# Optimization experiments

Hardware: AMD Instinct MI355X
Metric: run time of the kernel (lower is better)

The kernel has to match this reference:

```python
import jax, jax.numpy as jnp
import numpy as np

EPS = 1e-06        # normalize eps and log eps (module's self.eps)
PDIST_EPS = 1e-06  # torch.nn.PairwiseDistance default eps: ||x1 - x2 + eps||_2

A, C, F = 4096, 8, 64


def setup_inputs() -> dict:
    key = jax.random.key(0)
    x = jax.random.normal(key, (A, C, F), dtype=jnp.float32)
    return {"x": x}


def reference(x) -> jnp.ndarray:
    a = x.shape[0]
    c = x.shape[1]
    # F.normalize(p=2, dim=-1, eps=EPS): x / max(||x||_2, eps)
    nrm = jnp.linalg.norm(x, axis=-1, keepdims=True)
    xn = x / jnp.maximum(nrm, EPS)
    # pairwise cosine similarity per group: [C, A, A]
    sim = jnp.einsum('acf,bcf->cab', xn, xn)
    # mask self-similarity on the diagonal with -1
    diag = jnp.eye(a, dtype=bool)[None, :, :]
    sim = jnp.where(diag, -1.0, sim)
    # nearest neighbor per (c, a): argmax over b -> [C, A] -> [A, C]
    idx = jnp.argmax(sim, axis=-1).T
    # gather matched embeddings: x_match[a, c, f] = xn[idx[a, c], c, f]
    x_match = xn[idx, jnp.arange(c)[None, :], :]
    # PairwiseDistance(p=2, eps=1e-6): ||x - x_match + eps||_2 over last dim
    min_dist = jnp.linalg.norm(xn - x_match + PDIST_EPS, axis=-1)
    loss = -jnp.mean(jnp.log(min_dist + EPS))
    return loss
```

## Files before the change

kernel.cpp:

```cpp
#include <hip/hip_runtime.h>
#include <math.h>

#define AN 4096
#define CN 8
#define FN 64
#define ACN (AN*CN)

typedef __attribute__((ext_vector_type(8))) short bf16x8;
typedef __attribute__((ext_vector_type(4))) float f32x4;

__device__ inline unsigned short f2bf(float f) {
    unsigned u = __float_as_uint(f);
    unsigned r = ((u >> 16) & 1) + 0x7FFFu;
    return (unsigned short)((u + r) >> 16);
}

__global__ __launch_bounds__(256) void k1_normalize(const float* __restrict__ x,
                                                    unsigned short* __restrict__ xnb,
                                                    float* __restrict__ sc)
{
    int tid  = threadIdx.x;
    int grp  = tid >> 4;
    int slot = tid & 15;
    int V = blockIdx.x * 16 + grp;
    const float4 v = *(const float4*)(x + (size_t)V * FN + slot * 4);
    float ss = v.x*v.x + v.y*v.y + v.z*v.z + v.w*v.w;
    ss += __shfl_xor(ss, 1);
    ss += __shfl_xor(ss, 2);
    ss += __shfl_xor(ss, 4);
    ss += __shfl_xor(ss, 8);
    float s = 1.0f / fmaxf(sqrtf(ss), 1e-6f);
    if (slot == 0) sc[V] = s;
    ushort4 ob;
    ob.x = f2bf(v.x * s); ob.y = f2bf(v.y * s);
    ob.z = f2bf(v.z * s); ob.w = f2bf(v.w * s);
    int a = V >> 3, c = V & 7;
    *(ushort4*)(xnb + ((size_t)c * AN + a) * FN + slot * 4) = ob;
}

__global__ __launch_bounds__(256, 2) void k2_argmax(const unsigned short* __restrict__ xnb,
                                                    unsigned int* __restrict__ pP)
{
    __shared__ uint4 lds4[2 * 512];

    int blk  = blockIdx.x;
    int qtr  = blk & 3;
    int rt   = (blk >> 2) & 31;
    int c    = blk >> 7;
    int a0   = rt * 128;
    int q0   = qtr * 1024;

    int tid  = threadIdx.x;
    int lane = tid & 63;
    int w    = tid >> 6;
    int l15  = lane & 15;
    int quad = lane >> 4;

    const uint4* __restrict__ Xc4 = (const uint4*)(xnb + (size_t)c * AN * FN);
    const bf16x8* __restrict__ X8 = (const bf16x8*)Xc4;

    int sr  = tid >> 3;
    int sch = tid & 7;

    #pragma unroll
    for (int s = 0; s < 2; ++s) {
        int r = sr + 32 * s;
        lds4[r * 8 + (sch ^ (r & 7))] = Xc4[(size_t)(q0 + r) * 8 + sch];
    }

    int arow = a0 + w * 32 + l15;
    bf16x8 afr[2][2];
    #pragma unroll
    for (int mi = 0; mi < 2; ++mi)
        #pragma unroll
        for (int ks = 0; ks < 2; ++ks)
            afr[mi][ks] = X8[(size_t)(arow + mi * 16) * 8 + ks * 4 + quad];

    int rel   = (a0 + w * 32) - q0;
    int dit   = ((unsigned)rel < 1024u) ? (rel >> 6) : -1;
    int sdit  = __builtin_amdgcn_readfirstlane(dit);
    int nbase = __builtin_amdgcn_readfirstlane((rel >> 4) & 2);

    float bestp[8];
    #pragma unroll
    for (int i = 0; i < 8; ++i) bestp[i] = 0.0f;

    const f32x4 two = {2.0f, 2.0f, 2.0f, 2.0f};
    __syncthreads();

    #pragma unroll 2
    for (int it = 0; it < 16; ++it) {
        int cur = it & 1;

        uint4 gv[2];
        if (it < 15) {
            int g0 = q0 + (it + 1) * 64;
            #pragma unroll
            for (int s = 0; s < 2; ++s)
                gv[s] = Xc4[(size_t)(g0 + sr + 32 * s) * 8 + sch];
        }

        const bf16x8* bt = (const bf16x8*)(lds4 + cur * 512);
        bf16x8 bfr[2][4];
        #pragma unroll
        for (int ks = 0; ks < 2; ++ks)
            #pragma unroll
            for (int ni = 0; ni < 4; ++ni) {
                int r  = ni * 16 + l15;
                int ch = (ks * 4 + quad) ^ (r & 7);
                bfr[ks][ni] = bt[r * 8 + ch];
            }

        f32x4 acc[2][4];
        #pragma unroll
        for (int ni = 0; ni < 4; ++ni)
            #pragma unroll
            for (int mi = 0; mi < 2; ++mi) {
                acc[mi][ni] = __builtin_amdgcn_mfma_f32_16x16x32_bf16(afr[mi][0], bfr[0][ni], two, 0, 0, 0);
                acc[mi][ni] = __builtin_amdgcn_mfma_f32_16x16x32_bf16(afr[mi][1], bfr[1][ni], acc[mi][ni], 0, 0, 0);
            }

        if (it == sdit) {
            #pragma unroll
            for (int mi = 0; mi < 2; ++mi)
                #pragma unroll
                for (int rr = 0; rr < 4; ++rr)
                    if (l15 == quad * 4 + rr) acc[mi][nbase + mi][rr] = -2.0f;
        }

        #pragma unroll
        for (int mi = 0; mi < 2; ++mi)
            #pragma unroll
            for (int rr = 0; rr < 4; ++rr) {
                unsigned p0 = (__float_as_uint(acc[mi][0][rr]) & 0xFFFFF000u) | (unsigned)(it * 64);
                unsigned p1 = (__float_as_uint(acc[mi][1][rr]) & 0xFFFFF000u) | (unsigned)(it * 64 + 16);
                unsigned p2 = (__float_as_uint(acc[mi][2][rr]) & 0xFFFFF000u) | (unsigned)(it * 64 + 32);
                unsigned p3 = (__float_as_uint(acc[mi][3][rr]) & 0xFFFFF000u) | (unsigned)(it * 64 + 48);
                float m0 = fmaxf(fmaxf(__uint_as_float(p0), __uint_as_float(p1)), __uint_as_float(p2));
                bestp[mi * 4 + rr] = fmaxf(fmaxf(m0, __uint_as_float(p3)), bestp[mi * 4 + rr]);
            }

        if (it < 15) {
            #pragma unroll
            for (int s = 0; s < 2; ++s) {
                int r = sr + 32 * s;
                lds4[(cur ^ 1) * 512 + r * 8 + (sch ^ (r & 7))] = gv[s];
            }
        }
        __syncthreads();
    }

    unsigned tailcode = (unsigned)(q0 + l15);
    #pragma unroll
    for (int i = 0; i < 8; ++i) {
        float v = __uint_as_float(__float_as_uint(bestp[i]) | tailcode);
        v = fmaxf(v, __shfl_xor(v, 1));
        v = fmaxf(v, __shfl_xor(v, 2));
        v = fmaxf(v, __shfl_xor(v, 4));
        v = fmaxf(v, __shfl_xor(v, 8));
        bestp[i] = v;
    }
    if (l15 == 0) {
        #pragma unroll
        for (int mi = 0; mi < 2; ++mi)
            #pragma unroll
            for (int rr = 0; rr < 4; ++rr) {
                int a = a0 + w * 32 + mi * 16 + quad * 4 + rr;
                pP[(size_t)qtr * ACN + (size_t)a * CN + c] = __float_as_uint(bestp[mi * 4 + rr]);
            }
    }
}

__global__ __launch_bounds__(256) void k3_dist(const float* __restrict__ x,
                                               const float* __restrict__ sc,
                                               const unsigned int* __restrict__ pP,
                                               float* __restrict__ partials)
{
    int id = blockIdx.x * 256 + threadIdx.x;
    float p0 = __uint_as_float(pP[id]);
    float p1 = __uint_as_float(pP[ACN + id]);
    float p2 = __uint_as_float(pP[2 * ACN + id]);
    float p3 = __uint_as_float(pP[3 * ACN + id]);
    unsigned pm = __float_as_uint(fmaxf(fmaxf(p0, p1), fmaxf(p2, p3)));
    int m = (int)(pm & 0xFFFu);
    int c = id & 7;
    int jb = m * CN + c;
    float sa = sc[id], sb = sc[jb];
    const float* xa = x + (size_t)id * FN;
    const float* xb = x + (size_t)jb * FN;
    float ss = 0.0f;
    #pragma unroll
    for (int q = 0; q < 16; ++q) {
        float4 va = *(const float4*)(xa + 4 * q);
        float4 vb = *(const float4*)(xb + 4 * q);
        float d0 = va.x * sa - vb.x * sb + 1e-6f;
        float d1 = va.y * sa - vb.y * sb + 1e-6f;
        float d2 = va.z * sa - vb.z * sb + 1e-6f;
        float d3 = va.w * sa - vb.w * sb + 1e-6f;
        ss += d0*d0 + d1*d1 + d2*d2 + d3*d3;
    }
    float val = logf(sqrtf(ss) + 1e-6f);

    float t = val;
    #pragma unroll
    for (int off = 32; off > 0; off >>= 1) t += __shfl_down(t, off);
    __shared__ float ws4[4];
    if ((threadIdx.x & 63) == 0) ws4[threadIdx.x >> 6] = t;
    __syncthreads();
    if (threadIdx.x == 0)
        partials[blockIdx.x] = ws4[0] + ws4[1] + ws4[2] + ws4[3];
}

__global__ __launch_bounds__(64) void k4_final(const float* __restrict__ partials,
                                               float* __restrict__ out)
{
    int t = threadIdx.x;
    float v = partials[t] + partials[t + 64];
    #pragma unroll
    for (int off = 32; off > 0; off >>= 1) v += __shfl_down(v, off);
    if (t == 0) out[0] = -v / (float)ACN;
}

extern "C" void kernel_launch(void* const* d_in, const int* in_sizes, int n_in,
                              void* d_out, int out_size, void* d_ws, size_t ws_size,
                              hipStream_t stream)
{
    const float* x = (const float*)d_in[0];
    unsigned short* xnb = (unsigned short*)d_ws;
    float* sc = (float*)(xnb + (size_t)AN * CN * FN);
    unsigned int* pP = (unsigned int*)(sc + ACN);
    float* partials = (float*)(pP + 4 * ACN);

    k1_normalize<<<2048, 256, 0, stream>>>(x, xnb, sc);
    k2_argmax  <<<1024, 256, 0, stream>>>(xnb, pP);
    k3_dist    <<<128, 256, 0, stream>>>(x, sc, pP, partials);
    k4_final   <<<1, 64, 0, stream>>>(partials, (float*)d_out);
}
```

Baseline: 112.5 us.

## Load argmax B tiles directly from global memory, dropping LDS staging and barriers

The argmax kernel no longer stages 64-row B tiles through double-buffered swizzled LDS with per-iteration __syncthreads. Each wave now reads its B fragments straight from global memory, relying on L1/L2 caching because all four waves read the same rows. This removes the barrier and LDS traffic and allows higher occupancy by dropping the min-blocks hint. The cost is four times more global/L1 load requests and load latency that is no longer hidden by the software prefetch.

```diff
diff --git a/kernel.cpp b/kernel.cpp
--- a/kernel.cpp
+++ b/kernel.cpp
@@ -38,11 +38,9 @@
     *(ushort4*)(xnb + ((size_t)c * AN + a) * FN + slot * 4) = ob;
 }
 
-__global__ __launch_bounds__(256, 2) void k2_argmax(const unsigned short* __restrict__ xnb,
-                                                    unsigned int* __restrict__ pP)
-{
-    __shared__ uint4 lds4[2 * 512];
-
+__global__ __launch_bounds__(256) void k2_argmax(const unsigned short* __restrict__ xnb,
+                                                 unsigned int* __restrict__ pP)
+{
     int blk  = blockIdx.x;
     int qtr  = blk & 3;
     int rt   = (blk >> 2) & 31;
@@ -56,17 +54,7 @@
     int l15  = lane & 15;
     int quad = lane >> 4;
 
-    const uint4* __restrict__ Xc4 = (const uint4*)(xnb + (size_t)c * AN * FN);
-    const bf16x8* __restrict__ X8 = (const bf16x8*)Xc4;
-
-    int sr  = tid >> 3;
-    int sch = tid & 7;
-
-    #pragma unroll
-    for (int s = 0; s < 2; ++s) {
-        int r = sr + 32 * s;
-        lds4[r * 8 + (sch ^ (r & 7))] = Xc4[(size_t)(q0 + r) * 8 + sch];
-    }
+    const bf16x8* __restrict__ X8 = (const bf16x8*)(xnb + (size_t)c * AN * FN);
 
     int arow = a0 + w * 32 + l15;
     bf16x8 afr[2][2];
@@ -86,30 +74,16 @@
     for (int i = 0; i < 8; ++i) bestp[i] = 0.0f;
 
     const f32x4 two = {2.0f, 2.0f, 2.0f, 2.0f};
-    __syncthreads();
 
     #pragma unroll 2
     for (int it = 0; it < 16; ++it) {
-        int cur = it & 1;
-
-        uint4 gv[2];
-        if (it < 15) {
-            int g0 = q0 + (it + 1) * 64;
-            #pragma unroll
-            for (int s = 0; s < 2; ++s)
-                gv[s] = Xc4[(size_t)(g0 + sr + 32 * s) * 8 + sch];
-        }
-
-        const bf16x8* bt = (const bf16x8*)(lds4 + cur * 512);
+        int brow = q0 + it * 64 + l15;
         bf16x8 bfr[2][4];
         #pragma unroll
         for (int ks = 0; ks < 2; ++ks)
             #pragma unroll
-            for (int ni = 0; ni < 4; ++ni) {
-                int r  = ni * 16 + l15;
-                int ch = (ks * 4 + quad) ^ (r & 7);
-                bfr[ks][ni] = bt[r * 8 + ch];
-            }
+            for (int ni = 0; ni < 4; ++ni)
+                bfr[ks][ni] = X8[(size_t)(brow + ni * 16) * 8 + ks * 4 + quad];
 
         f32x4 acc[2][4];
         #pragma unroll
@@ -139,15 +113,6 @@
                 float m0 = fmaxf(fmaxf(__uint_as_float(p0), __uint_as_float(p1)), __uint_as_float(p2));
                 bestp[mi * 4 + rr] = fmaxf(fmaxf(m0, __uint_as_float(p3)), bestp[mi * 4 + rr]);
             }
-
-        if (it < 15) {
-            #pragma unroll
-            for (int s = 0; s < 2; ++s) {
-                int r = sr + 32 * s;
-                lds4[(cur ^ 1) * 512 + r * 8 + (sch ^ (r & 7))] = gv[s];
-            }
-        }
-        __syncthreads();
     }
 
     unsigned tailcode = (unsigned)(q0 + l15);
```

After: 133.1 us. 18.4% more time.
